# Kernel tuning notes

Measured on AMD Instinct MI355X. Metric: run time of the kernel, lower is better.

Reference implementation:

```python
import math
import jax, jax.numpy as jnp
import numpy as np

B, T, C, H, DQK, DV = 2, 2048, 1024, 16, 64, 64


def setup_inputs() -> dict:
    key = jax.random.key(0)
    ks = jax.random.split(key, 5)
    x = jax.random.normal(ks[0], (B, T, C), dtype=jnp.float32)
    # randw: randn(*d) / sqrt(d[-1])
    w_q = jax.random.normal(ks[1], (H, DQK, C), dtype=jnp.float32) / math.sqrt(C)
    w_k = jax.random.normal(ks[2], (H, DQK, C), dtype=jnp.float32) / math.sqrt(C)
    w_v = jax.random.normal(ks[3], (H, DV, C), dtype=jnp.float32) / math.sqrt(C)
    w_o = jax.random.normal(ks[4], (DV * H, C), dtype=jnp.float32) / math.sqrt(C)
    return {"x": x, "w_q": w_q, "w_k": w_k, "w_v": w_v, "w_o": w_o}


def reference(x, w_q, w_k, w_v, w_o):
    # Full-sequence causal forward (bs_q.first == 0, nb == T): caches are
    # fully written in one shot, so they reduce to the plain projections.
    n, t, c = x.shape
    q = jnp.einsum('ntc,hdc->nhtd', x, w_q)
    k = jnp.einsum('ntc,hdc->nhtd', x, w_k)
    v = jnp.einsum('ntc,hdc->nhtd', x, w_v)
    scale = 1.0 / math.sqrt(w_q.shape[1])
    a = jnp.einsum('nhtd,nhsd->nhts', q, k) * scale  # [n,h,t,s]
    causal = jnp.arange(t)[:, None] < jnp.arange(t)[None, :]  # True above diag
    a = jnp.where(causal[None, None, :, :], -jnp.inf, a)
    a = jax.nn.softmax(a, axis=3)
    y = jnp.einsum('nhts,nhsd->nthd', a, v).reshape(n, t, -1)  # [n,t,h*dv]
    return y @ w_o  # cache_y, [n,t,c]
```

## Files before the change

### kernel.cpp

```cpp
#include <hip/hip_runtime.h>


typedef short bf16x4 __attribute__((ext_vector_type(4)));
typedef short bf16x8 __attribute__((ext_vector_type(8)));
typedef float f32x4 __attribute__((ext_vector_type(4)));

#define MFMA_BF16 __builtin_amdgcn_mfma_f32_16x16x32_bf16

#define QSCALE 0.18033688011112042f

__device__ __forceinline__ unsigned short f2bf(float f) {
    union { float f; unsigned u; } un; un.f = f;
    unsigned r = un.u + 0x7fffu + ((un.u >> 16) & 1u);
    return (unsigned short)(r >> 16);
}
__device__ __forceinline__ unsigned pk2(float a, float b) {
    return (unsigned)f2bf(a) | ((unsigned)f2bf(b) << 16);
}
__device__ __forceinline__ unsigned pk2t(float a, float b) {
    union { float f; unsigned u; } ua, ub; ua.f = a; ub.f = b;
    return (ua.u >> 16) | (ub.u & 0xffff0000u);
}
__device__ __forceinline__ void gload16(const void* g, void* l) {
    __builtin_amdgcn_global_load_lds(
        (const __attribute__((address_space(1))) unsigned int*)g,
        (__attribute__((address_space(3))) unsigned int*)l, 16, 0, 0);
}

__global__ __launch_bounds__(256) void prep(
    const float* __restrict__ x, const float* __restrict__ wq,
    const float* __restrict__ wk, const float* __restrict__ wv,
    const float* __restrict__ wo,
    unsigned short* __restrict__ x16, unsigned short* __restrict__ wq16,
    unsigned short* __restrict__ wk16, unsigned short* __restrict__ wv16,
    unsigned short* __restrict__ wot)
{
    const int bid = blockIdx.x;
    if (bid < 3584) {
        const float* s; unsigned short* d; int off;
        if (bid < 2048)      { s = x;  d = x16;  off = bid * 2048; }
        else if (bid < 2560) { s = wq; d = wq16; off = (bid - 2048) * 2048; }
        else if (bid < 3072) { s = wk; d = wk16; off = (bid - 2560) * 2048; }
        else                 { s = wv; d = wv16; off = (bid - 3072) * 2048; }
        int i = off + threadIdx.x * 8;
        float4 f0 = *(const float4*)&s[i], f1 = *(const float4*)&s[i + 4];
        uint4 o;
        o.x = pk2(f0.x, f0.y); o.y = pk2(f0.z, f0.w);
        o.z = pk2(f1.x, f1.y); o.w = pk2(f1.z, f1.w);
        *(uint4*)&d[i] = o;
    } else {
        __shared__ unsigned short t[64 * 72];
        const int b2 = bid - 3584;
        const int k0 = (b2 & 15) << 6, n0 = (b2 >> 4) << 6;
        const int r = threadIdx.x >> 2, cg = (threadIdx.x & 3) << 4;
        const float* src = &wo[(k0 + r) * 1024 + n0 + cg];
        #pragma unroll
        for (int j = 0; j < 16; j += 4) {
            float4 f = *(const float4*)&src[j];
            t[(cg + j + 0) * 72 + r] = f2bf(f.x);
            t[(cg + j + 1) * 72 + r] = f2bf(f.y);
            t[(cg + j + 2) * 72 + r] = f2bf(f.z);
            t[(cg + j + 3) * 72 + r] = f2bf(f.w);
        }
        __syncthreads();
        unsigned short* dst = &wot[(n0 + r) * 1024 + k0 + cg];
        unsigned short* tr = &t[r * 72 + cg];
        unsigned v[16];
        #pragma unroll
        for (int j = 0; j < 16; ++j) v[j] = tr[j];
        uint4 o0, o1;
        o0.x = v[0] | (v[1] << 16);   o0.y = v[2] | (v[3] << 16);
        o0.z = v[4] | (v[5] << 16);   o0.w = v[6] | (v[7] << 16);
        o1.x = v[8] | (v[9] << 16);   o1.y = v[10] | (v[11] << 16);
        o1.z = v[12] | (v[13] << 16); o1.w = v[14] | (v[15] << 16);
        *(uint4*)&dst[0] = o0;
        *(uint4*)&dst[8] = o1;
    }
}

__device__ __forceinline__ void gemm_body(
    const unsigned short* __restrict__ A, const unsigned short* __restrict__ Bm,
    void* __restrict__ C, int m0, int n0, int mode, int ldc, float sc)
{
    __shared__ unsigned short sa[2][128 * 32];
    __shared__ unsigned short sb[2][128 * 32];
    const int tid = threadIdx.x, wave = tid >> 6, lane = tid & 63;
    const int l15 = lane & 15, l4 = lane >> 4;
    const int wm = (wave >> 1) << 6, wn = (wave & 1) << 6;

    const int r16 = lane >> 2;
    const int gcol = (((lane & 3) ^ ((r16 >> 1) & 3)) << 3);
    const int rcol = (l4 ^ ((l15 >> 1) & 3)) << 3;
    const unsigned short* Ag0 = &A[(size_t)(m0 + wave * 16 + r16) * 1024 + gcol];
    const unsigned short* Ag1 = Ag0 + (size_t)64 * 1024;
    const unsigned short* Bg0 = &Bm[(size_t)(n0 + wave * 16 + r16) * 1024 + gcol];
    const unsigned short* Bg1 = Bg0 + (size_t)64 * 1024;
    const int lb0 = (wave * 16) * 32;
    const int lb1 = (64 + wave * 16) * 32;

    gload16(Ag0, &sa[0][lb0]);
    gload16(Ag1, &sa[0][lb1]);
    gload16(Bg0, &sb[0][lb0]);
    gload16(Bg1, &sb[0][lb1]);
    __syncthreads();

    f32x4 acc[4][4] = {};

    #pragma unroll
    for (int kk = 0; kk < 32; ++kk) {
        const int cur = kk & 1;
        if (kk < 31) {
            const int off = (kk + 1) * 32;
            const int nxt = 1 - cur;
            gload16(Ag0 + off, &sa[nxt][lb0]);
            gload16(Ag1 + off, &sa[nxt][lb1]);
            gload16(Bg0 + off, &sb[nxt][lb0]);
            gload16(Bg1 + off, &sb[nxt][lb1]);
        }
        bf16x8 af[4], bf4[4];
        #pragma unroll
        for (int i = 0; i < 4; ++i)
            af[i] = *(const bf16x8*)&sa[cur][(wm + i * 16 + l15) * 32 + rcol];
        #pragma unroll
        for (int j = 0; j < 4; ++j)
            bf4[j] = *(const bf16x8*)&sb[cur][(wn + j * 16 + l15) * 32 + rcol];
        #pragma unroll
        for (int i = 0; i < 4; ++i)
            #pragma unroll
            for (int j = 0; j < 4; ++j)
                acc[i][j] = MFMA_BF16(af[i], bf4[j], acc[i][j], 0, 0, 0);
        __syncthreads();
    }

    #pragma unroll
    for (int i = 0; i < 4; ++i)
        #pragma unroll
        for (int j = 0; j < 4; ++j)
            #pragma unroll
            for (int r = 0; r < 4; ++r) {
                int row = m0 + wm + i * 16 + l4 * 4 + r;
                int col = n0 + wn + j * 16 + l15;
                float val = acc[i][j][r];
                if (mode == 0) {
                    int nb = row >> 11, t = row & 2047;
                    int hh = col >> 6, dd = col & 63;
                    ((unsigned short*)C)[(((nb << 4) + hh) * 2048 + t) * 64 + dd] =
                        f2bf(val * sc);
                } else if (mode == 1) {
                    ((float*)C)[(size_t)row * ldc + col] = val;
                } else {
                    int s = col & 31;
                    int cp = (col & ~31) | (((s >> 2) & 3) << 3)
                                         | (((s >> 4) & 1) << 2) | (s & 3);
                    ((unsigned short*)C)[(size_t)row * ldc + cp] = f2bf(val);
                }
            }
}

__global__ __launch_bounds__(256) void proj(
    const unsigned short* __restrict__ x16,
    const unsigned short* __restrict__ wq16,
    const unsigned short* __restrict__ wk16,
    const unsigned short* __restrict__ wv16,
    unsigned short* __restrict__ qbuf,
    unsigned short* __restrict__ kbuf,
    unsigned short* __restrict__ vtb)
{
    const int bid = blockIdx.x;
    if (bid < 512) {
        int m0 = (bid & 31) << 7;
        int n0g = (bid >> 5) << 7;
        if (n0g < 1024)
            gemm_body(x16, wq16, qbuf, m0, n0g, 0, 0, QSCALE);
        else
            gemm_body(x16, wk16, kbuf, m0, n0g - 1024, 0, 0, 1.0f);
    } else {
        int v = bid - 512;
        gemm_body(wv16, x16, vtb, (v & 7) << 7, (v >> 3) << 7, 2, 4096, 1.0f);
    }
}

__global__ __launch_bounds__(256) void outp(
    const unsigned short* __restrict__ ybuf,
    const unsigned short* __restrict__ wot,
    float* __restrict__ out)
{
    __shared__ unsigned short sa[2][64 * 32];
    __shared__ unsigned short sb[2][64 * 32];
    const int tid = threadIdx.x, wave = tid >> 6, lane = tid & 63;
    const int l15 = lane & 15, l4 = lane >> 4;
    const int bid = blockIdx.x;
    const int m0 = (bid & 63) << 6, n0 = (bid >> 6) << 6;

    const int r16 = lane >> 2;
    const int gcol = (((lane & 3) ^ ((r16 >> 1) & 3)) << 3);
    const int rcol = (l4 ^ ((l15 >> 1) & 3)) << 3;
    const unsigned short* Ag = &ybuf[(size_t)(m0 + wave * 16 + r16) * 1024 + gcol];
    const unsigned short* Bg = &wot[(size_t)(n0 + wave * 16 + r16) * 1024 + gcol];
    const int lb = (wave * 16) * 32;

    gload16(Ag, &sa[0][lb]);
    gload16(Bg, &sb[0][lb]);
    __syncthreads();

    f32x4 acc[4] = {};

    #pragma unroll
    for (int kk = 0; kk < 32; ++kk) {
        const int cur = kk & 1;
        if (kk < 31) {
            const int off = (kk + 1) * 32;
            gload16(Ag + off, &sa[1 - cur][lb]);
            gload16(Bg + off, &sb[1 - cur][lb]);
        }
        bf16x8 af = *(const bf16x8*)&sa[cur][(wave * 16 + l15) * 32 + rcol];
        #pragma unroll
        for (int j = 0; j < 4; ++j) {
            bf16x8 bf = *(const bf16x8*)&sb[cur][(j * 16 + l15) * 32 + rcol];
            acc[j] = MFMA_BF16(af, bf, acc[j], 0, 0, 0);
        }
        __syncthreads();
    }

    #pragma unroll
    for (int j = 0; j < 4; ++j)
        #pragma unroll
        for (int r = 0; r < 4; ++r) {
            int row = m0 + wave * 16 + l4 * 4 + r;
            int col = n0 + j * 16 + l15;
            out[(size_t)row * 1024 + col] = acc[j][r];
        }
}

__global__ __launch_bounds__(256) void attn(
    const unsigned short* __restrict__ q,
    const unsigned short* __restrict__ k,
    const unsigned short* __restrict__ vt,
    unsigned short* __restrict__ y)
{
    __shared__ unsigned short sk[2][64 * 64];
    __shared__ unsigned short sv[2][64 * 64];
    const int tid = threadIdx.x, wave = tid >> 6, lane = tid & 63;
    const int l15 = lane & 15, l4 = lane >> 4;
    const int bid = blockIdx.x;
    const int qtt = (bid < 512) ? (31 - (bid >> 5)) : ((bid - 512) >> 5);
    const int bh = bid & 31;
    const int nb = bh >> 4, hh = bh & 15;
    const int q0 = qtt << 6;
    const size_t base = (size_t)bh << 17;

    const int lrow = lane >> 3;
    const int gch = ((lane & 7) ^ lrow) << 3;
    const int row0 = wave * 8 + lrow, row1 = 32 + wave * 8 + lrow;
    const unsigned short* kg0 = &k[base + (size_t)row0 * 64 + gch];
    const unsigned short* kg1 = &k[base + (size_t)row1 * 64 + gch];
    const unsigned short* vg0 = &vt[(size_t)((hh << 6) + row0) * 4096 + (nb << 11) + gch];
    const unsigned short* vg1 = &vt[(size_t)((hh << 6) + row1) * 4096 + (nb << 11) + gch];
    const int lbk0 = (wave * 8) * 64, lbk1 = (32 + wave * 8) * 64;

    bf16x8 qf[2];
    #pragma unroll
    for (int ks = 0; ks < 2; ++ks)
        qf[ks] = *(const bf16x8*)
            &q[base + (size_t)(q0 + wave * 16 + l15) * 64 + ks * 32 + l4 * 8];

    float l_sum = 0.f;
    f32x4 acc[4] = {};

    const int nst = qtt + 1;

    const int rch0 = ((0 + l4) ^ (l15 & 7)) << 3;
    const int rch1 = ((4 + l4) ^ (l15 & 7)) << 3;

    gload16(kg0, &sk[0][lbk0]);
    gload16(kg1, &sk[0][lbk1]);
    gload16(vg0, &sv[0][lbk0]);
    gload16(vg1, &sv[0][lbk1]);
    __syncthreads();

    auto step = [&](const int cur, const int st, const bool more) {
        if (more) {
            const int nxt = cur ^ 1;
            const int s1e = (st + 1) << 6;
            gload16(kg0 + ((size_t)s1e << 6), &sk[nxt][lbk0]);
            gload16(kg1 + ((size_t)s1e << 6), &sk[nxt][lbk1]);
            gload16(vg0 + s1e, &sv[nxt][lbk0]);
            gload16(vg1 + s1e, &sv[nxt][lbk1]);
        }

        f32x4 s_acc[4] = {};
        #pragma unroll
        for (int ns = 0; ns < 4; ++ns) {
            bf16x8 kf0 = *(const bf16x8*)&sk[cur][(ns * 16 + l15) * 64 + rch0];
            bf16x8 kf1 = *(const bf16x8*)&sk[cur][(ns * 16 + l15) * 64 + rch1];
            s_acc[ns] = MFMA_BF16(kf0, qf[0], s_acc[ns], 0, 0, 0);
            s_acc[ns] = MFMA_BF16(kf1, qf[1], s_acc[ns], 0, 0, 0);
        }

        if (st == qtt) {
            const int ql = wave * 16 + l15;
            #pragma unroll
            for (int ns = 0; ns < 4; ++ns) {
                #pragma unroll
                for (int r = 0; r < 4; ++r)
                    if (ns * 16 + l4 * 4 + r > ql) s_acc[ns][r] = -1e30f;
            }
        }

        float pe[4][4];
        #pragma unroll
        for (int ns = 0; ns < 4; ++ns) {
            #pragma unroll
            for (int r = 0; r < 4; ++r) pe[ns][r] = exp2f(s_acc[ns][r]);
            l_sum += (pe[ns][0] + pe[ns][1]) + (pe[ns][2] + pe[ns][3]);
        }

        #pragma unroll
        for (int ks = 0; ks < 2; ++ks) {
            uint4 pw;
            pw.x = pk2t(pe[2 * ks][0], pe[2 * ks][1]);
            pw.y = pk2t(pe[2 * ks][2], pe[2 * ks][3]);
            pw.z = pk2t(pe[2 * ks + 1][0], pe[2 * ks + 1][1]);
            pw.w = pk2t(pe[2 * ks + 1][2], pe[2 * ks + 1][3]);
            bf16x8 pf = *(bf16x8*)&pw;
            const int rch = ks ? rch1 : rch0;
            #pragma unroll
            for (int ds = 0; ds < 4; ++ds) {
                bf16x8 vf = *(const bf16x8*)&sv[cur][(ds * 16 + l15) * 64 + rch];
                acc[ds] = MFMA_BF16(vf, pf, acc[ds], 0, 0, 0);
            }
        }
        __syncthreads();
    };

    int st = 0;
    for (; st + 2 <= nst; st += 2) {
        step(0, st, true);
        step(1, st + 1, (st + 2) < nst);
    }
    if (st < nst) step(0, st, false);

    l_sum += __shfl_xor(l_sum, 16);
    l_sum += __shfl_xor(l_sum, 32);
    const float rl = __builtin_amdgcn_rcpf(l_sum);

    const size_t rowbase =
        ((size_t)((nb << 11) + q0 + wave * 16 + l15) << 10) + (hh << 6) + l4 * 4;
    #pragma unroll
    for (int ds = 0; ds < 4; ++ds) {
        uint2 o;
        o.x = pk2(acc[ds][0] * rl, acc[ds][1] * rl);
        o.y = pk2(acc[ds][2] * rl, acc[ds][3] * rl);
        *(uint2*)&y[rowbase + ds * 16] = o;
    }
}

extern "C" void kernel_launch(void* const* d_in, const int* in_sizes, int n_in,
                              void* d_out, int out_size, void* d_ws, size_t ws_size,
                              hipStream_t stream) {
    const float* x  = (const float*)d_in[0];
    const float* wq = (const float*)d_in[1];
    const float* wk = (const float*)d_in[2];
    const float* wv = (const float*)d_in[3];
    const float* wo = (const float*)d_in[4];
    float* out = (float*)d_out;

    const size_t M1 = 1u << 20;
    unsigned short* x16  = (unsigned short*)d_ws;
    unsigned short* wq16 = x16 + 4 * M1;
    unsigned short* wk16 = wq16 + M1;
    unsigned short* wv16 = wk16 + M1;
    unsigned short* wot  = wv16 + M1;
    unsigned short* qbuf = wot + M1;
    unsigned short* kbuf = qbuf + 4 * M1;
    unsigned short* vtb  = kbuf + 4 * M1;
    unsigned short* ybuf = vtb + 4 * M1;

    dim3 blk(256);
    prep<<<3840, blk, 0, stream>>>(x, wq, wk, wv, wo, x16, wq16, wk16, wv16, wot);
    proj<<<768, blk, 0, stream>>>(x16, wq16, wk16, wv16, qbuf, kbuf, vtb);
    attn<<<1024, blk, 0, stream>>>(qbuf, kbuf, vtb, ybuf);
    outp<<<1024, blk, 0, stream>>>(ybuf, wot, out);
}
```

Before: 171.0 us.

## Process two query tiles per attention block and reuse gemm_body for output projection

```diff
diff --git a/kernel.cpp b/kernel.cpp
--- a/kernel.cpp
+++ b/kernel.cpp
@@ -185,51 +185,8 @@
     const unsigned short* __restrict__ wot,
     float* __restrict__ out)
 {
-    __shared__ unsigned short sa[2][64 * 32];
-    __shared__ unsigned short sb[2][64 * 32];
-    const int tid = threadIdx.x, wave = tid >> 6, lane = tid & 63;
-    const int l15 = lane & 15, l4 = lane >> 4;
     const int bid = blockIdx.x;
-    const int m0 = (bid & 63) << 6, n0 = (bid >> 6) << 6;
-
-    const int r16 = lane >> 2;
-    const int gcol = (((lane & 3) ^ ((r16 >> 1) & 3)) << 3);
-    const int rcol = (l4 ^ ((l15 >> 1) & 3)) << 3;
-    const unsigned short* Ag = &ybuf[(size_t)(m0 + wave * 16 + r16) * 1024 + gcol];
-    const unsigned short* Bg = &wot[(size_t)(n0 + wave * 16 + r16) * 1024 + gcol];
-    const int lb = (wave * 16) * 32;
-
-    gload16(Ag, &sa[0][lb]);
-    gload16(Bg, &sb[0][lb]);
-    __syncthreads();
-
-    f32x4 acc[4] = {};
-
-    #pragma unroll
-    for (int kk = 0; kk < 32; ++kk) {
-        const int cur = kk & 1;
-        if (kk < 31) {
-            const int off = (kk + 1) * 32;
-            gload16(Ag + off, &sa[1 - cur][lb]);
-            gload16(Bg + off, &sb[1 - cur][lb]);
-        }
-        bf16x8 af = *(const bf16x8*)&sa[cur][(wave * 16 + l15) * 32 + rcol];
-        #pragma unroll
-        for (int j = 0; j < 4; ++j) {
-            bf16x8 bf = *(const bf16x8*)&sb[cur][(j * 16 + l15) * 32 + rcol];
-            acc[j] = MFMA_BF16(af, bf, acc[j], 0, 0, 0);
-        }
-        __syncthreads();
-    }
-
-    #pragma unroll
-    for (int j = 0; j < 4; ++j)
-        #pragma unroll
-        for (int r = 0; r < 4; ++r) {
-            int row = m0 + wave * 16 + l4 * 4 + r;
-            int col = n0 + j * 16 + l15;
-            out[(size_t)row * 1024 + col] = acc[j][r];
-        }
+    gemm_body(ybuf, wot, out, (bid & 31) << 7, (bid >> 5) << 7, 1, 1024, 1.0f);
 }
 
 __global__ __launch_bounds__(256) void attn(
@@ -243,10 +200,10 @@
     const int tid = threadIdx.x, wave = tid >> 6, lane = tid & 63;
     const int l15 = lane & 15, l4 = lane >> 4;
     const int bid = blockIdx.x;
-    const int qtt = (bid < 512) ? (31 - (bid >> 5)) : ((bid - 512) >> 5);
+    const int qtt = 15 - (bid >> 5);
     const int bh = bid & 31;
     const int nb = bh >> 4, hh = bh & 15;
-    const int q0 = qtt << 6;
+    const int q0 = qtt << 7;
     const size_t base = (size_t)bh << 17;
 
     const int lrow = lane >> 3;
@@ -258,16 +215,18 @@
     const unsigned short* vg1 = &vt[(size_t)((hh << 6) + row1) * 4096 + (nb << 11) + gch];
     const int lbk0 = (wave * 8) * 64, lbk1 = (32 + wave * 8) * 64;
 
-    bf16x8 qf[2];
+    bf16x8 qf[2][2];
     #pragma unroll
-    for (int ks = 0; ks < 2; ++ks)
-        qf[ks] = *(const bf16x8*)
-            &q[base + (size_t)(q0 + wave * 16 + l15) * 64 + ks * 32 + l4 * 8];
-
-    float l_sum = 0.f;
-    f32x4 acc[4] = {};
-
-    const int nst = qtt + 1;
+    for (int g = 0; g < 2; ++g)
+        #pragma unroll
+        for (int ks = 0; ks < 2; ++ks)
+            qf[g][ks] = *(const bf16x8*)
+                &q[base + (size_t)(q0 + (g << 6) + wave * 16 + l15) * 64 + ks * 32 + l4 * 8];
+
+    float l_sum[2] = {0.f, 0.f};
+    f32x4 acc[2][4] = {};
+
+    const int nst = 2 * qtt + 2;
 
     const int rch0 = ((0 + l4) ^ (l15 & 7)) << 3;
     const int rch1 = ((4 + l4) ^ (l15 & 7)) << 3;
@@ -288,46 +247,65 @@
             gload16(vg1 + s1e, &sv[nxt][lbk1]);
         }
 
-        f32x4 s_acc[4] = {};
+        f32x4 s_acc[2][4] = {};
         #pragma unroll
         for (int ns = 0; ns < 4; ++ns) {
             bf16x8 kf0 = *(const bf16x8*)&sk[cur][(ns * 16 + l15) * 64 + rch0];
             bf16x8 kf1 = *(const bf16x8*)&sk[cur][(ns * 16 + l15) * 64 + rch1];
-            s_acc[ns] = MFMA_BF16(kf0, qf[0], s_acc[ns], 0, 0, 0);
-            s_acc[ns] = MFMA_BF16(kf1, qf[1], s_acc[ns], 0, 0, 0);
-        }
-
-        if (st == qtt) {
-            const int ql = wave * 16 + l15;
+            s_acc[0][ns] = MFMA_BF16(kf0, qf[0][0], s_acc[0][ns], 0, 0, 0);
+            s_acc[0][ns] = MFMA_BF16(kf1, qf[0][1], s_acc[0][ns], 0, 0, 0);
+            s_acc[1][ns] = MFMA_BF16(kf0, qf[1][0], s_acc[1][ns], 0, 0, 0);
+            s_acc[1][ns] = MFMA_BF16(kf1, qf[1][1], s_acc[1][ns], 0, 0, 0);
+        }
+
+        if (st >= nst - 2) {
+            const int sb = st << 6;
+            #pragma unroll
+            for (int g = 0; g < 2; ++g) {
+                const int qlg = q0 + (g << 6) + wave * 16 + l15;
+                #pragma unroll
+                for (int ns = 0; ns < 4; ++ns)
+                    #pragma unroll
+                    for (int r = 0; r < 4; ++r)
+                        if (sb + ns * 16 + l4 * 4 + r > qlg) s_acc[g][ns][r] = -1e30f;
+            }
+        }
+
+        float pe[2][4][4];
+        #pragma unroll
+        for (int g = 0; g < 2; ++g)
             #pragma unroll
             for (int ns = 0; ns < 4; ++ns) {
                 #pragma unroll
-                for (int r = 0; r < 4; ++r)
-                    if (ns * 16 + l4 * 4 + r > ql) s_acc[ns][r] = -1e30f;
-            }
-        }
-
-        float pe[4][4];
-        #pragma unroll
-        for (int ns = 0; ns < 4; ++ns) {
-            #pragma unroll
-            for (int r = 0; r < 4; ++r) pe[ns][r] = exp2f(s_acc[ns][r]);
-            l_sum += (pe[ns][0] + pe[ns][1]) + (pe[ns][2] + pe[ns][3]);
-        }
+                for (int r = 0; r < 4; ++r) pe[g][ns][r] = exp2f(s_acc[g][ns][r]);
+                l_sum[g] += (pe[g][ns][0] + pe[g][ns][1]) + (pe[g][ns][2] + pe[g][ns][3]);
+            }
 
         #pragma unroll
         for (int ks = 0; ks < 2; ++ks) {
-            uint4 pw;
-            pw.x = pk2t(pe[2 * ks][0], pe[2 * ks][1]);
-            pw.y = pk2t(pe[2 * ks][2], pe[2 * ks][3]);
-            pw.z = pk2t(pe[2 * ks + 1][0], pe[2 * ks + 1][1]);
-            pw.w = pk2t(pe[2 * ks + 1][2], pe[2 * ks + 1][3]);
-            bf16x8 pf = *(bf16x8*)&pw;
+            bf16x8 pf0, pf1;
+            {
+                uint4 pw;
+                pw.x = pk2t(pe[0][2 * ks][0], pe[0][2 * ks][1]);
+                pw.y = pk2t(pe[0][2 * ks][2], pe[0][2 * ks][3]);
+                pw.z = pk2t(pe[0][2 * ks + 1][0], pe[0][2 * ks + 1][1]);
+                pw.w = pk2t(pe[0][2 * ks + 1][2], pe[0][2 * ks + 1][3]);
+                pf0 = *(bf16x8*)&pw;
+            }
+            {
+                uint4 pw;
+                pw.x = pk2t(pe[1][2 * ks][0], pe[1][2 * ks][1]);
+                pw.y = pk2t(pe[1][2 * ks][2], pe[1][2 * ks][3]);
+                pw.z = pk2t(pe[1][2 * ks + 1][0], pe[1][2 * ks + 1][1]);
+                pw.w = pk2t(pe[1][2 * ks + 1][2], pe[1][2 * ks + 1][3]);
+                pf1 = *(bf16x8*)&pw;
+            }
             const int rch = ks ? rch1 : rch0;
             #pragma unroll
             for (int ds = 0; ds < 4; ++ds) {
                 bf16x8 vf = *(const bf16x8*)&sv[cur][(ds * 16 + l15) * 64 + rch];
-                acc[ds] = MFMA_BF16(vf, pf, acc[ds], 0, 0, 0);
+                acc[0][ds] = MFMA_BF16(vf, pf0, acc[0][ds], 0, 0, 0);
+                acc[1][ds] = MFMA_BF16(vf, pf1, acc[1][ds], 0, 0, 0);
             }
         }
         __syncthreads();
@@ -340,18 +318,22 @@
     }
     if (st < nst) step(0, st, false);
 
-    l_sum += __shfl_xor(l_sum, 16);
-    l_sum += __shfl_xor(l_sum, 32);
-    const float rl = __builtin_amdgcn_rcpf(l_sum);
-
-    const size_t rowbase =
-        ((size_t)((nb << 11) + q0 + wave * 16 + l15) << 10) + (hh << 6) + l4 * 4;
     #pragma unroll
-    for (int ds = 0; ds < 4; ++ds) {
-        uint2 o;
-        o.x = pk2(acc[ds][0] * rl, acc[ds][1] * rl);
-        o.y = pk2(acc[ds][2] * rl, acc[ds][3] * rl);
-        *(uint2*)&y[rowbase + ds * 16] = o;
+    for (int g = 0; g < 2; ++g) {
+        float ls = l_sum[g];
+        ls += __shfl_xor(ls, 16);
+        ls += __shfl_xor(ls, 32);
+        const float rl = __builtin_amdgcn_rcpf(ls);
+
+        const size_t rowbase =
+            ((size_t)((nb << 11) + q0 + (g << 6) + wave * 16 + l15) << 10) + (hh << 6) + l4 * 4;
+        #pragma unroll
+        for (int ds = 0; ds < 4; ++ds) {
+            uint2 o;
+            o.x = pk2(acc[g][ds][0] * rl, acc[g][ds][1] * rl);
+            o.y = pk2(acc[g][ds][2] * rl, acc[g][ds][3] * rl);
+            *(uint2*)&y[rowbase + ds * 16] = o;
+        }
     }
 }
 
@@ -379,6 +361,6 @@
     dim3 blk(256);
     prep<<<3840, blk, 0, stream>>>(x, wq, wk, wv, wo, x16, wq16, wk16, wv16, wot);
     proj<<<768, blk, 0, stream>>>(x16, wq16, wk16, wv16, qbuf, kbuf, vtb);
-    attn<<<1024, blk, 0, stream>>>(qbuf, kbuf, vtb, ybuf);
-    outp<<<1024, blk, 0, stream>>>(ybuf, wot, out);
-}
+    attn<<<512, blk, 0, stream>>>(qbuf, kbuf, vtb, ybuf);
+    outp<<<256, blk, 0, stream>>>(ybuf, wot, out);
+}
```

New measurement: 176.6 us. 3.2% more time.
